# Optimization experiments

Hardware: AMD Instinct MI355X
Metric: run time of the kernel (lower is better)

Reference implementation:

```python
import jax, jax.numpy as jnp
import numpy as np

N_NODES = 100000
N_EDGES = 1600000
IN_DIM = 128
HID = 256
N_GRAPHS = 256
N_OUT = 2


def setup_inputs() -> dict:
    key = jax.random.key(0)
    ks = jax.random.split(key, 16)
    s_in = 1.0 / np.sqrt(IN_DIM)
    s_h = 1.0 / np.sqrt(HID)
    return {
        "x": jax.random.normal(ks[0], (N_NODES, IN_DIM), jnp.float32),
        "W_pool": jax.random.normal(ks[1], (IN_DIM, IN_DIM), jnp.float32) * s_in,
        "b_pool": jnp.zeros((IN_DIM,), jnp.float32),
        "W_self": jax.random.normal(ks[2], (IN_DIM, HID), jnp.float32) * s_in,
        "W_neigh": jax.random.normal(ks[3], (IN_DIM, HID), jnp.float32) * s_in,
        "b_sage": jnp.zeros((HID,), jnp.float32),
        "W1": jax.random.normal(ks[4], (HID, HID), jnp.float32) * s_h,
        "b1": jnp.zeros((HID,), jnp.float32),
        "W2": jax.random.normal(ks[5], (HID, HID), jnp.float32) * s_h,
        "b2": jnp.zeros((HID,), jnp.float32),
        "Wr": jax.random.normal(ks[6], (HID, N_OUT), jnp.float32) * s_h,
        "br": jnp.zeros((N_OUT,), jnp.float32),
        "src": jax.random.randint(ks[7], (N_EDGES,), 0, N_NODES, jnp.int32),
        "dst": jax.random.randint(ks[8], (N_EDGES,), 0, N_NODES, jnp.int32),
        "graph_id": jnp.sort(jax.random.randint(ks[9], (N_NODES,), 0, N_GRAPHS, jnp.int32)),
    }


def reference(x, W_pool, b_pool, W_self, W_neigh, b_sage, W1, b1, W2, b2, Wr, br, src, dst, graph_id):
    n = x.shape[0]
    # --- SAGEConv 'pool' aggregator ---
    m = jax.nn.relu(x @ W_pool + b_pool)                      # [N, IN]
    neigh = jax.ops.segment_max(m[src], dst, num_segments=n)  # max over in-neighbors
    neigh = jnp.where(jnp.isfinite(neigh), neigh, 0.0)        # isolated nodes -> 0 (DGL zero-init)
    h = jax.nn.relu(x @ W_self + neigh @ W_neigh + b_sage)    # [N, HID]
    # --- MLP stack ---
    h = jax.nn.relu(h @ W1 + b1)
    h = jax.nn.relu(h @ W2 + b2)
    # --- softmax_nodes: per-graph softmax over nodes, per feature ---
    gmax = jax.ops.segment_max(h, graph_id, num_segments=N_GRAPHS)
    gmax = jnp.where(jnp.isfinite(gmax), gmax, 0.0)
    z = jnp.exp(h - gmax[graph_id])                           # [N, HID]
    zsum = jax.ops.segment_sum(z, graph_id, num_segments=N_GRAPHS)
    hg = z / zsum[graph_id]
    # --- max_nodes readout ---
    final = jax.ops.segment_max(hg, graph_id, num_segments=N_GRAPHS)
    final = jnp.where(jnp.isfinite(final), final, 0.0)        # [G, HID]
    return final @ Wr + br                                    # [G, N_OUT]
```

## Files before the change

kernel.cpp:

```cpp
#include <hip/hip_runtime.h>

#define N_NODES  100000
#define N_EDGES  1600000
#define IN_DIM   128
#define HID      256
#define N_GRAPHS 256
#define ESHIFT   20.0f
#define BSH      7
#define NB2      782

typedef _Float16 f16x8 __attribute__((ext_vector_type(8)));
typedef float f32x16 __attribute__((ext_vector_type(16)));
#define MFMA16(a, b, c) __builtin_amdgcn_mfma_f32_32x32x16_f16((a), (b), (c), 0, 0, 0)

#define PKMAX(a, b) asm("v_pk_max_f16 %0, %0, %1" : "+v"(a) : "v"(b))

#define BARX() __builtin_amdgcn_s_barrier()
#define WAITVM(N) asm volatile("s_waitcnt vmcnt(" #N ")" ::: "memory")

static __device__ __forceinline__ unsigned short f2h_bits(float f) {
    _Float16 h = (_Float16)f;
    return __builtin_bit_cast(unsigned short, h);
}
static __device__ __forceinline__ float h2f(unsigned short b) {
    return (float)__builtin_bit_cast(_Float16, b);
}

static __device__ __forceinline__ void decode_blk(int M, int& m0, int& n0)
{
    const int gmb = (M + 127) >> 7;
    const int l = blockIdx.x;
    int mb, nb;
    if ((int)gridDim.x == gmb) {
        mb = l; nb = 0;
    } else {
        const int nfull = (gmb >> 3) << 4;
        if (l < nfull) {
            mb = ((l >> 4) << 3) | (l & 7);
            nb = (l >> 3) & 1;
        } else {
            const int t = l - nfull, tm = gmb & 7;
            mb = (gmb & ~7) + (t % tm);
            nb = t / tm;
        }
    }
    m0 = mb * 128;
    n0 = nb * 128;
}

__global__ __launch_bounds__(256) void x_to_h(
    const float* __restrict__ in, unsigned short* __restrict__ xh, int n)
{
    int i = (blockIdx.x * 256 + threadIdx.x) * 4;
    if (i < n) {
        float4 v = *(const float4*)&in[i];
        ushort4 h;
        h.x = f2h_bits(v.x); h.y = f2h_bits(v.y);
        h.z = f2h_bits(v.z); h.w = f2h_bits(v.w);
        *(ushort4*)&xh[i] = h;
    }
}

__global__ __launch_bounds__(256) void w_split_h(
    const float* __restrict__ Wa, const float* __restrict__ Wb, int K1,
    int K, int N, unsigned short* __restrict__ hi, unsigned short* __restrict__ lo)
{
    int idx = blockIdx.x * 256 + threadIdx.x;
    if (idx >= K * N) return;
    int k = idx / N, n = idx - k * N;
    float w = (k < K1) ? Wa[(size_t)k * N + n] : Wb[(size_t)(k - K1) * N + n];
    unsigned short h = f2h_bits(w);
    unsigned short l = f2h_bits(w - h2f(h));
    hi[(size_t)n * K + k] = h;
    lo[(size_t)n * K + k] = l;
}

__global__ __launch_bounds__(256) void gemm_mfma_h(
    const unsigned short* __restrict__ A1, const unsigned short* __restrict__ A2,
    int K1, int Ktot,
    const unsigned short* __restrict__ Wh, const unsigned short* __restrict__ Wl,
    const float* __restrict__ bias, void* __restrict__ Cv,
    int M, int N, int mode)
{
    __shared__ __align__(16) short tA [128][32];
    __shared__ __align__(16) short tBh[128][32];
    __shared__ __align__(16) short tBl[128][32];

    const int tid  = threadIdx.x;
    int m0, n0;
    decode_blk(M, m0, n0);
    const int wave = tid >> 6, lane = tid & 63;
    const int mw   = (wave & 1) * 64, nw = (wave >> 1) * 64;
    const int lm   = lane & 31;

    const int rsub = lane >> 2;
    const int kqe  = ((lane & 3) ^ ((lane >> 3) & 3)) << 3;
    const int rw   = wave << 5;

    const int s4  = (lm >> 1) & 3;
    const int cB  = lane >> 5;
    const int ch0 = ((cB ^ s4) << 3);
    const int ch1 = (((2 | cB) ^ s4) << 3);
    const f16x8* a00 = (const f16x8*)&tA [mw + lm     ][ch0];
    const f16x8* a01 = (const f16x8*)&tA [mw + lm     ][ch1];
    const f16x8* a10 = (const f16x8*)&tA [mw + 32 + lm][ch0];
    const f16x8* a11 = (const f16x8*)&tA [mw + 32 + lm][ch1];
    const f16x8* bh00 = (const f16x8*)&tBh[nw + lm     ][ch0];
    const f16x8* bh01 = (const f16x8*)&tBh[nw + lm     ][ch1];
    const f16x8* bh10 = (const f16x8*)&tBh[nw + 32 + lm][ch0];
    const f16x8* bh11 = (const f16x8*)&tBh[nw + 32 + lm][ch1];
    const f16x8* bl00 = (const f16x8*)&tBl[nw + lm     ][ch0];
    const f16x8* bl01 = (const f16x8*)&tBl[nw + lm     ][ch1];
    const f16x8* bl10 = (const f16x8*)&tBl[nw + 32 + lm][ch0];
    const f16x8* bl11 = (const f16x8*)&tBl[nw + 32 + lm][ch1];

    f32x16 acc[4];
#pragma unroll
    for (int t = 0; t < 4; ++t)
#pragma unroll
        for (int i = 0; i < 16; ++i) acc[t][i] = 0.f;

    for (int kc = 0; kc < Ktot; kc += 32) {
        const unsigned short* Ab; int Astr, kl;
        if (kc < K1) { Ab = A1; Astr = K1;        kl = kc; }
        else         { Ab = A2; Astr = Ktot - K1; kl = kc - K1; }

        __syncthreads();
#pragma unroll
        for (int j = 0; j < 2; ++j) {
            const int tr = rw + j * 16;
            int row = m0 + tr + rsub; if (row >= M) row = M - 1;
            __builtin_amdgcn_global_load_lds(
                Ab + (size_t)row * Astr + kl + kqe, &tA[tr][0], 16, 0, 0);
            const size_t o = (size_t)(n0 + tr + rsub) * Ktot + kc + kqe;
            __builtin_amdgcn_global_load_lds(Wh + o, &tBh[tr][0], 16, 0, 0);
            __builtin_amdgcn_global_load_lds(Wl + o, &tBl[tr][0], 16, 0, 0);
        }
        __syncthreads();

        {
            f16x8 A0 = *a00, A1f = *a10;
            f16x8 B0h = *bh00, B1h = *bh10, B0l = *bl00, B1l = *bl10;
            acc[0] = MFMA16(A0,  B0h, acc[0]);
            acc[1] = MFMA16(A0,  B1h, acc[1]);
            acc[2] = MFMA16(A1f, B0h, acc[2]);
            acc[3] = MFMA16(A1f, B1h, acc[3]);
            acc[0] = MFMA16(A0,  B0l, acc[0]);
            acc[1] = MFMA16(A0,  B1l, acc[1]);
            acc[2] = MFMA16(A1f, B0l, acc[2]);
            acc[3] = MFMA16(A1f, B1l, acc[3]);
        }
        {
            f16x8 A0 = *a01, A1f = *a11;
            f16x8 B0h = *bh01, B1h = *bh11, B0l = *bl01, B1l = *bl11;
            acc[0] = MFMA16(A0,  B0h, acc[0]);
            acc[1] = MFMA16(A0,  B1h, acc[1]);
            acc[2] = MFMA16(A1f, B0h, acc[2]);
            acc[3] = MFMA16(A1f, B1h, acc[3]);
            acc[0] = MFMA16(A0,  B0l, acc[0]);
            acc[1] = MFMA16(A0,  B1l, acc[1]);
            acc[2] = MFMA16(A1f, B0l, acc[2]);
            acc[3] = MFMA16(A1f, B1l, acc[3]);
        }
    }

    const int rb = 4 * (lane >> 5);
#pragma unroll
    for (int ti = 0; ti < 2; ++ti)
#pragma unroll
    for (int tj = 0; tj < 2; ++tj) {
        f32x16 a = acc[ti * 2 + tj];
        int coln = n0 + nw + tj * 32 + lm;
        float bv = bias[coln];
#pragma unroll
        for (int reg = 0; reg < 16; ++reg) {
            int rrow = m0 + mw + ti * 32 + (reg & 3) + 8 * (reg >> 2) + rb;
            if (rrow < M) {
                float v = a[reg] + bv;
                v = v > 0.f ? v : 0.f;
                size_t o = (size_t)rrow * N + coln;
                if (mode == 0) ((float*)Cv)[o] = v;
                else           ((unsigned short*)Cv)[o] = f2h_bits(v);
            }
        }
    }
}

static __device__ __forceinline__ void stage_tile64(
    const unsigned short* __restrict__ A1, const unsigned short* __restrict__ A2,
    int K1, int M, int r0g, short* bufb, int wave, int lane)
{
    const int l5 = lane >> 5;
    const int s  = lane & 31;
#pragma unroll
    for (int i = 0; i < 4; ++i) {
        const int p    = wave * 4 + i;
        const int rloc = 2 * p + l5;
        int row = r0g + rloc; if (row >= M) row = M - 1;
        const int c8 = ((s ^ ((2 * i + l5) & 7)) << 3);
        const unsigned short* sp = (c8 < K1)
            ? A1 + (size_t)row * K1 + c8
            : A2 + (size_t)row * (256 - K1) + (c8 - K1);
        __builtin_amdgcn_global_load_lds(sp, bufb + p * 512, 16, 0, 0);
    }
}

__global__ __launch_bounds__(512, 2) void gemm_bstat(
    const unsigned short* __restrict__ A1, const unsigned short* __restrict__ A2,
    int K1,
    const unsigned short* __restrict__ Wh, const unsigned short* __restrict__ Wl,
    const float* __restrict__ bias, unsigned short* __restrict__ C,
    unsigned short* __restrict__ dummy, int M)
{
    __shared__ __align__(16) short buf[2][64][256];

    const int tid = threadIdx.x, wave = tid >> 6, lane = tid & 63;
    const int lm = lane & 31, hib = lane >> 5;
    const int col = wave * 32 + lm;
    const int hi8 = hib * 8;

    f16x8 Bh[16], Bl[16];
#pragma unroll
    for (int k = 0; k < 16; ++k) {
        const size_t o = (size_t)col * 256 + k * 16 + hi8;
        Bh[k] = *(const f16x8*)(Wh + o);
        Bl[k] = *(const f16x8*)(Wl + o);
    }

    const int nt = (M + 63) >> 6;
    const int G = gridDim.x, b = blockIdx.x;
    const int q = nt / G, r = nt % G;
    const int t0  = b * q + (b < r ? b : r);
    const int ntl = q + (b < r ? 1 : 0);

    const int rq    = (lm >> 1) & 3;
    const int abase = lm * 512 + ((hib ^ (lm & 1)) << 4);
    const float bv  = bias[col];
    const int rb    = 4 * hib;

    stage_tile64(A1, A2, K1, M, t0 << 6, &buf[0][0][0], wave, lane);
    if (ntl > 1)
        stage_tile64(A1, A2, K1, M, (t0 + 1) << 6, &buf[1][0][0], wave, lane);

    for (int t = 0; t < ntl; ++t) {
        if (t == 0) { if (ntl > 1) WAITVM(4); else WAITVM(0); }
        else if (t + 1 < ntl) WAITVM(36);
        else WAITVM(32);
        BARX();

        f32x16 acc0, acc1;
#pragma unroll
        for (int i = 0; i < 16; ++i) { acc0[i] = 0.f; acc1[i] = 0.f; }
        const char* lb = (const char*)&buf[t & 1][0][0];
#pragma unroll
        for (int k = 0; k < 16; ++k) {
            const int koff = ((k ^ rq) << 5);
            f16x8 a0 = *(const f16x8*)(lb + abase + koff);
            f16x8 a1 = *(const f16x8*)(lb + abase + koff + 16384);
            acc0 = MFMA16(a0, Bh[k], acc0);
            acc1 = MFMA16(a1, Bh[k], acc1);
            acc0 = MFMA16(a0, Bl[k], acc0);
            acc1 = MFMA16(a1, Bl[k], acc1);
        }
        BARX();

        if (t + 2 < ntl)
            stage_tile64(A1, A2, K1, M, (t0 + t + 2) << 6,
                         &buf[t & 1][0][0], wave, lane);
        const int r0g = (t0 + t) << 6;
#pragma unroll
        for (int reg = 0; reg < 16; ++reg) {
            const int rr0 = r0g + (reg & 3) + 8 * (reg >> 2) + rb;
            const int rr1 = rr0 + 32;
            unsigned short* d0 = (rr0 < M) ? C + (size_t)rr0 * 256 + col : dummy + tid;
            unsigned short* d1 = (rr1 < M) ? C + (size_t)rr1 * 256 + col : dummy + tid;
            *d0 = f2h_bits(fmaxf(acc0[reg] + bv, 0.f));
            *d1 = f2h_bits(fmaxf(acc1[reg] + bv, 0.f));
        }
    }
}

static __device__ __forceinline__ void sm_flush(
    int run_g, float run_s, float run_m, int gfirst, int col,
    float* sS, int* sM, float* ps, float* pm)
{
    if (run_g < 0) return;
    int slot = run_g - gfirst;
    if (slot < 8) {
        atomicAdd(&sS[slot * 256 + col], run_s);
        atomicMax(&sM[slot * 256 + col], __float_as_int(run_m));
    } else {
        atomicAdd(&ps[(size_t)run_g * HID + col], run_s);
        atomicMax((int*)&pm[(size_t)run_g * HID + col], __float_as_int(run_m));
    }
}

__global__ __launch_bounds__(512, 2) void gemm_bstat_sm(
    const unsigned short* __restrict__ A,
    const unsigned short* __restrict__ Wh, const unsigned short* __restrict__ Wl,
    const float* __restrict__ bias, const int* __restrict__ gid,
    float* __restrict__ pm, float* __restrict__ ps, int M)
{
    __shared__ __align__(16) short buf[2][64][256];
    __shared__ float sS[8 * 256];
    __shared__ int   sM[8 * 256];

    const int tid = threadIdx.x, wave = tid >> 6, lane = tid & 63;
    const int lm = lane & 31, hib = lane >> 5;
    const int col = wave * 32 + lm;
    const int hi8 = hib * 8;

    for (int i = tid; i < 2048; i += 512) { sS[i] = 0.f; sM[i] = 0; }

    f16x8 Bh[16], Bl[16];
#pragma unroll
    for (int k = 0; k < 16; ++k) {
        const size_t o = (size_t)col * 256 + k * 16 + hi8;
        Bh[k] = *(const f16x8*)(Wh + o);
        Bl[k] = *(const f16x8*)(Wl + o);
    }

    const int nt = (M + 63) >> 6;
    const int G = gridDim.x, b = blockIdx.x;
    const int q = nt / G, r = nt % G;
    const int t0  = b * q + (b < r ? b : r);
    const int ntl = q + (b < r ? 1 : 0);

    const int rq    = (lm >> 1) & 3;
    const int abase = lm * 512 + ((hib ^ (lm & 1)) << 4);
    const float bv  = bias[col];
    const int rb    = 4 * hib;
    const int gfirst = gid[t0 << 6];

    stage_tile64(A, A, 256, M, t0 << 6, &buf[0][0][0], wave, lane);
    if (ntl > 1)
        stage_tile64(A, A, 256, M, (t0 + 1) << 6, &buf[1][0][0], wave, lane);

    int run_g = -1; float run_s = 0.f, run_m = 0.f;

    for (int t = 0; t < ntl; ++t) {
        if (t + 1 < ntl) WAITVM(4); else WAITVM(0);
        BARX();

        const int r0g = (t0 + t) << 6;
        int gr = r0g + lane; if (gr >= M) gr = M - 1;
        int gv = gid[gr];
        asm volatile("" :: "v"(gv));

        f32x16 acc0, acc1;
#pragma unroll
        for (int i = 0; i < 16; ++i) { acc0[i] = 0.f; acc1[i] = 0.f; }
        const char* lb = (const char*)&buf[t & 1][0][0];
#pragma unroll
        for (int k = 0; k < 16; ++k) {
            const int koff = ((k ^ rq) << 5);
            f16x8 a0 = *(const f16x8*)(lb + abase + koff);
            f16x8 a1 = *(const f16x8*)(lb + abase + koff + 16384);
            acc0 = MFMA16(a0, Bh[k], acc0);
            acc1 = MFMA16(a1, Bh[k], acc1);
            acc0 = MFMA16(a0, Bl[k], acc0);
            acc1 = MFMA16(a1, Bl[k], acc1);
        }
        BARX();

        if (t + 2 < ntl) {
            stage_tile64(A, A, 256, M, (t0 + t + 2) << 6,
                         &buf[t & 1][0][0], wave, lane);
            WAITVM(4);
        } else {
            WAITVM(0);
        }

        const int gT0 = __shfl(gv, 0);
        const int gT1 = __shfl(gv, 63);
        if (gT0 == gT1) {
            if (gT0 != run_g) {
                sm_flush(run_g, run_s, run_m, gfirst, col, sS, sM, ps, pm);
                run_g = gT0; run_s = 0.f; run_m = 0.f;
            }
#pragma unroll
            for (int sub = 0; sub < 2; ++sub) {
                const f32x16& a = sub ? acc1 : acc0;
#pragma unroll
                for (int reg = 0; reg < 16; ++reg) {
                    const int rrow = r0g + sub * 32 + (reg & 3) + 8 * (reg >> 2) + rb;
                    float v = fmaxf(a[reg] + bv, 0.f);
                    bool ok = rrow < M;
                    run_s += ok ? __expf(v - ESHIFT) : 0.f;
                    run_m = ok ? fmaxf(run_m, v) : run_m;
                }
            }
        } else {
#pragma unroll
            for (int sub = 0; sub < 2; ++sub) {
                const f32x16& a = sub ? acc1 : acc0;
#pragma unroll
                for (int reg = 0; reg < 16; ++reg) {
                    const int roff = sub * 32 + (reg & 3) + 8 * (reg >> 2) + rb;
                    const int rrow = r0g + roff;
                    int g = __shfl(gv, roff);
                    if (rrow >= M) continue;
                    float v = fmaxf(a[reg] + bv, 0.f);
                    if (g != run_g) {
                        sm_flush(run_g, run_s, run_m, gfirst, col, sS, sM, ps, pm);
                        run_g = g; run_s = 0.f; run_m = 0.f;
                    }
                    run_s += __expf(v - ESHIFT);
                    run_m = fmaxf(run_m, v);
                }
            }
        }
    }

    sm_flush(run_g, run_s, run_m, gfirst, col, sS, sM, ps, pm);
    __syncthreads();

    int lastrow = ((t0 + ntl) << 6) - 1; if (lastrow >= M) lastrow = M - 1;
    int span = gid[lastrow] - gfirst + 1; if (span > 8) span = 8;
    for (int i = tid; i < span * 256; i += 512) {
        float vs = sS[i];
        if (vs > 0.f) {
            int g = gfirst + (i >> 8), c = i & 255;
            atomicAdd(&ps[(size_t)g * HID + c], vs);
            atomicMax((int*)&pm[(size_t)g * HID + c], sM[i]);
        }
    }
}

__global__ __launch_bounds__(256) void part_count(
    const int* __restrict__ dst, int* __restrict__ btot, int E)
{
    __shared__ int sh[NB2];
    const int t = threadIdx.x;
    for (int i = t; i < NB2; i += 256) sh[i] = 0;
    __syncthreads();
    int base = blockIdx.x * 4096 + t;
#pragma unroll
    for (int i = 0; i < 16; ++i) {
        int e = base + i * 256;
        if (e < E) atomicAdd(&sh[dst[e] >> BSH], 1);
    }
    __syncthreads();
    for (int i = t; i < NB2; i += 256)
        if (sh[i]) atomicAdd(&btot[i], sh[i]);
}

__global__ __launch_bounds__(256) void scan_b(
    const int* __restrict__ btot, int* __restrict__ bstart,
    int* __restrict__ cursor, int total)
{
    __shared__ int sh[256];
    const int t = threadIdx.x;
    int a[4];
    int s = 0;
#pragma unroll
    for (int i = 0; i < 4; ++i) {
        int idx = t * 4 + i;
        a[i] = (idx < NB2) ? btot[idx] : 0;
        s += a[i];
    }
    sh[t] = s;
    __syncthreads();
    for (int off = 1; off < 256; off <<= 1) {
        int v = (t >= off) ? sh[t - off] : 0;
        __syncthreads();
        if (t >= off) sh[t] += v;
        __syncthreads();
    }
    int run = (t > 0) ? sh[t - 1] : 0;
#pragma unroll
    for (int i = 0; i < 4; ++i) {
        int idx = t * 4 + i;
        if (idx < NB2) { bstart[idx] = run; cursor[idx] = run; }
        run += a[i];
    }
    if (t == 0) bstart[NB2] = total;
}

__global__ __launch_bounds__(256) void part_scatter(
    const int* __restrict__ src, const int* __restrict__ dst,
    int* __restrict__ cursor, int2* __restrict__ pairs, int E)
{
    __shared__ int cnt[NB2], goff[NB2], fill[NB2];
    const int t = threadIdx.x;
    const int base = blockIdx.x * 4096;
    for (int i = t; i < NB2; i += 256) { cnt[i] = 0; fill[i] = 0; }
    __syncthreads();
    int myd[16];
#pragma unroll
    for (int i = 0; i < 16; ++i) {
        int e = base + t + i * 256;
        myd[i] = (e < E) ? dst[e] : -1;
        if (myd[i] >= 0) atomicAdd(&cnt[myd[i] >> BSH], 1);
    }
    __syncthreads();
    for (int i = t; i < NB2; i += 256)
        goff[i] = cnt[i] ? atomicAdd(&cursor[i], cnt[i]) : 0;
    __syncthreads();
#pragma unroll
    for (int i = 0; i < 16; ++i) {
        int e = base + t + i * 256;
        if (myd[i] >= 0) {
            int b = myd[i] >> BSH;
            int r = atomicAdd(&fill[b], 1);
            pairs[goff[b] + r] = make_int2(myd[i], src[e]);
        }
    }
}

__global__ __launch_bounds__(256) void bucket_sort(
    const int2* __restrict__ pairs, const int* __restrict__ bstart,
    int* __restrict__ csr_src, int* __restrict__ offs, int Nn, int E)
{
    __shared__ int cnt[128], off[128];
    const int b = blockIdx.x;
    const int t = threadIdx.x;
    const int lo = bstart[b], hi = bstart[b + 1];
    if (t < 128) cnt[t] = 0;
    __syncthreads();
    for (int e = lo + t; e < hi; e += 256)
        atomicAdd(&cnt[pairs[e].x & 127], 1);
    __syncthreads();
    if (t == 0) {
        int s = 0;
        for (int i = 0; i < 128; ++i) { off[i] = s; s += cnt[i]; }
    }
    __syncthreads();
    if (t < 128) {
        int node = (b << BSH) + t;
        if (node < Nn) offs[node] = lo + off[t];
        cnt[t] = off[t];
    }
    if (b == NB2 - 1 && t == 0) offs[Nn] = E;
    __syncthreads();
    for (int e = lo + t; e < hi; e += 256) {
        int2 p = pairs[e];
        int r = atomicAdd(&cnt[p.x & 127], 1);
        csr_src[lo + r] = p.y;
    }
}

__global__ __launch_bounds__(256) void csr_max_agg_h(
    const unsigned short* __restrict__ m, const int* __restrict__ csr_src,
    const int* __restrict__ offs, unsigned short* __restrict__ neigh, int Nn)
{
    const int node = (blockIdx.x * 256 + threadIdx.x) >> 6;
    const int lane = threadIdx.x & 63;
    if (node >= Nn) return;
    const int e0  = offs[node];
    const int end = offs[node + 1];
    const char* mc = (const char*)m;

    uint4 a0 = make_uint4(0u, 0u, 0u, 0u);
    uint4 a1 = a0, a2 = a0, a3 = a0;
    if (end > e0) {
        const unsigned fo = (unsigned)(lane & 15) << 4;
        const int sub = lane >> 4;
        for (int base = e0; base < end; base += 64) {
            int ee = base + lane;
            int sl = csr_src[ee < end ? ee : (end - 1)];
            int cnt = end - base; if (cnt > 64) cnt = 64;
            int iters = (cnt + 3) >> 2;
            for (int j = 0; j < iters; j += 4) {
                int j1 = j + 1 < 16 ? j + 1 : 15;
                int j2 = j + 2 < 16 ? j + 2 : 15;
                int j3 = j + 3 < 16 ? j + 3 : 15;
                int s0 = __shfl(sl, (j  << 2) | sub);
                int s1 = __shfl(sl, (j1 << 2) | sub);
                int s2 = __shfl(sl, (j2 << 2) | sub);
                int s3 = __shfl(sl, (j3 << 2) | sub);
                uint4 v0 = *(const uint4*)(mc + (((unsigned)s0 << 8) | fo));
                uint4 v1 = *(const uint4*)(mc + (((unsigned)s1 << 8) | fo));
                uint4 v2 = *(const uint4*)(mc + (((unsigned)s2 << 8) | fo));
                uint4 v3 = *(const uint4*)(mc + (((unsigned)s3 << 8) | fo));
                PKMAX(a0.x, v0.x); PKMAX(a0.y, v0.y);
                PKMAX(a0.z, v0.z); PKMAX(a0.w, v0.w);
                PKMAX(a1.x, v1.x); PKMAX(a1.y, v1.y);
                PKMAX(a1.z, v1.z); PKMAX(a1.w, v1.w);
                PKMAX(a2.x, v2.x); PKMAX(a2.y, v2.y);
                PKMAX(a2.z, v2.z); PKMAX(a2.w, v2.w);
                PKMAX(a3.x, v3.x); PKMAX(a3.y, v3.y);
                PKMAX(a3.z, v3.z); PKMAX(a3.w, v3.w);
            }
        }
        PKMAX(a0.x, a1.x); PKMAX(a0.y, a1.y);
        PKMAX(a0.z, a1.z); PKMAX(a0.w, a1.w);
        PKMAX(a2.x, a3.x); PKMAX(a2.y, a3.y);
        PKMAX(a2.z, a3.z); PKMAX(a2.w, a3.w);
        PKMAX(a0.x, a2.x); PKMAX(a0.y, a2.y);
        PKMAX(a0.z, a2.z); PKMAX(a0.w, a2.w);
        uint4 o;
        o.x = __shfl_xor(a0.x, 16); o.y = __shfl_xor(a0.y, 16);
        o.z = __shfl_xor(a0.z, 16); o.w = __shfl_xor(a0.w, 16);
        PKMAX(a0.x, o.x); PKMAX(a0.y, o.y);
        PKMAX(a0.z, o.z); PKMAX(a0.w, o.w);
        o.x = __shfl_xor(a0.x, 32); o.y = __shfl_xor(a0.y, 32);
        o.z = __shfl_xor(a0.z, 32); o.w = __shfl_xor(a0.w, 32);
        PKMAX(a0.x, o.x); PKMAX(a0.y, o.y);
        PKMAX(a0.z, o.z); PKMAX(a0.w, o.w);
    }
    if (lane < 16)
        *(uint4*)((char*)neigh + (((size_t)node << 8) | ((unsigned)lane << 4))) = a0;
}

__global__ __launch_bounds__(256) void softmax_merge(
    const float* __restrict__ pm, const float* __restrict__ ps,
    const float* __restrict__ Wr, const float* __restrict__ brv,
    float* __restrict__ out)
{
    const int g = blockIdx.x;
    const int j = threadIdx.x;

    float M = pm[(size_t)g * HID + j];
    float S = ps[(size_t)g * HID + j];
    float fm = (S > 0.f) ? __expf(M - ESHIFT) / S : 0.f;

    float p0 = fm * Wr[j * 2 + 0];
    float p1 = fm * Wr[j * 2 + 1];
#pragma unroll
    for (int off = 32; off > 0; off >>= 1) {
        p0 += __shfl_down(p0, off);
        p1 += __shfl_down(p1, off);
    }
    __shared__ float red[8];
    int wv = j >> 6, ln = j & 63;
    if (ln == 0) { red[wv * 2] = p0; red[wv * 2 + 1] = p1; }
    __syncthreads();
    if (j == 0) out[g * 2 + 0] = red[0] + red[2] + red[4] + red[6] + brv[0];
    if (j == 1) out[g * 2 + 1] = red[1] + red[3] + red[5] + red[7] + brv[1];
}

extern "C" void kernel_launch(void* const* d_in, const int* in_sizes, int n_in,
                              void* d_out, int out_size, void* d_ws, size_t ws_size,
                              hipStream_t stream)
{
    const float* x      = (const float*)d_in[0];
    const float* W_pool = (const float*)d_in[1];
    const float* b_pool = (const float*)d_in[2];
    const float* W_self = (const float*)d_in[3];
    const float* W_neigh= (const float*)d_in[4];
    const float* b_sage = (const float*)d_in[5];
    const float* W1     = (const float*)d_in[6];
    const float* b1     = (const float*)d_in[7];
    const float* W2     = (const float*)d_in[8];
    const float* b2     = (const float*)d_in[9];
    const float* Wr     = (const float*)d_in[10];
    const float* br     = (const float*)d_in[11];
    const int*   src    = (const int*)d_in[12];
    const int*   dst    = (const int*)d_in[13];
    const int*   gid    = (const int*)d_in[14];

    const int Nn = N_NODES, E = N_EDGES;
    char* ws = (char*)d_ws;

    unsigned short* xh    = (unsigned short*)(ws + 0);
    unsigned short* m_buf = (unsigned short*)(ws + 25600000);
    unsigned short* neigh = (unsigned short*)(ws + 51200000);
    int2*           pairs = (int2*)(ws + 76800000);
    int*            btot  = (int*)(ws + 89600000);
    int*            bstart= btot + NB2;
    int*            cursor= bstart + NB2 + 1;
    float*          pm    = (float*)(ws + 90000000);
    float*          ps    = pm + (size_t)N_GRAPHS * HID;
    int*            offs  = (int*)(ws + 91000000);
    int*            csr_src = (int*)(ws + 91500000);
    unsigned short* h1    = (unsigned short*)(ws + 102400000);
    unsigned short* h2    = (unsigned short*)(ws + 153600000);
    unsigned short* dummy = (unsigned short*)pairs;

    char* srcws = (char*)(void*)src;
    unsigned short* wpool_h = (unsigned short*)(srcws + 0);
    unsigned short* wpool_l = wpool_h + 128 * 128;
    unsigned short* wsage_h = wpool_l + 128 * 128;
    unsigned short* wsage_l = wsage_h + 256 * 256;
    unsigned short* w1_h    = wsage_l + 256 * 256;
    unsigned short* w1_l    = w1_h + 256 * 256;
    unsigned short* w2_h    = w1_l + 256 * 256;
    unsigned short* w2_l    = w2_h + 256 * 256;

    dim3 blk(256);
    const int gm = (Nn + 127) / 128;
    const int pchunks = (E + 4095) / 4096;

    hipMemsetAsync(btot, 0, NB2 * sizeof(int), stream);
    hipMemsetAsync(pm, 0, (size_t)2 * N_GRAPHS * HID * sizeof(float), stream);

    x_to_h<<<dim3((Nn * IN_DIM / 4 + 255) / 256), blk, 0, stream>>>(
        x, xh, Nn * IN_DIM);

    part_count<<<dim3(pchunks), blk, 0, stream>>>(dst, btot, E);
    scan_b<<<dim3(1), blk, 0, stream>>>(btot, bstart, cursor, E);
    part_scatter<<<dim3(pchunks), blk, 0, stream>>>(src, dst, cursor, pairs, E);
    bucket_sort<<<dim3(NB2), blk, 0, stream>>>(pairs, bstart, csr_src, offs, Nn, E);

    w_split_h<<<dim3((128 * 128 + 255) / 256), blk, 0, stream>>>(
        W_pool, W_pool, 128, 128, 128, wpool_h, wpool_l);
    w_split_h<<<dim3((256 * 256 + 255) / 256), blk, 0, stream>>>(
        W_self, W_neigh, 128, 256, 256, wsage_h, wsage_l);
    w_split_h<<<dim3((256 * 256 + 255) / 256), blk, 0, stream>>>(
        W1, W1, 256, 256, 256, w1_h, w1_l);
    w_split_h<<<dim3((256 * 256 + 255) / 256), blk, 0, stream>>>(
        W2, W2, 256, 256, 256, w2_h, w2_l);

    gemm_mfma_h<<<dim3(gm), blk, 0, stream>>>(
        xh, xh, 128, 128, wpool_h, wpool_l, b_pool, m_buf, Nn, 128, 1);

    csr_max_agg_h<<<dim3((Nn * 64 + 255) / 256), blk, 0, stream>>>(
        m_buf, csr_src, offs, neigh, Nn);

    gemm_bstat<<<dim3(256), dim3(512), 0, stream>>>(
        xh, neigh, 128, wsage_h, wsage_l, b_sage, h1, dummy, Nn);

    gemm_bstat<<<dim3(256), dim3(512), 0, stream>>>(
        h1, h1, 256, w1_h, w1_l, b1, h2, dummy, Nn);

    gemm_bstat_sm<<<dim3(256), dim3(512), 0, stream>>>(
        h2, w2_h, w2_l, b2, gid, pm, ps, Nn);

    softmax_merge<<<dim3(N_GRAPHS), blk, 0, stream>>>(pm, ps, Wr, br, (float*)d_out);
}
```

Before: 411.8 us.

## Fuse prep kernels and use persistent register-resident-weight GEMM for pool layer

Merges the x-to-fp16 conversion with the edge-bucket counting into one launch, and the four weight-split launches into one. It also replaces the generic LDS-tiled GEMM for the pool projection with a persistent 256-block kernel. That kernel keeps the 128x128 hi/lo weights in registers and double-buffers 64-row A tiles through LDS. The aim is to cut launch overhead and the redundant weight loads per tile in the first GEMM, at the cost of higher register pressure and manual vmcnt bookkeeping.

```diff
diff --git a/kernel.cpp b/kernel.cpp
--- a/kernel.cpp
+++ b/kernel.cpp
@@ -8,6 +8,7 @@
 #define ESHIFT   20.0f
 #define BSH      7
 #define NB2      782
+#define XHB      12500
 
 typedef _Float16 f16x8 __attribute__((ext_vector_type(8)));
 typedef float f32x16 __attribute__((ext_vector_type(16)));
@@ -26,46 +27,41 @@
     return (float)__builtin_bit_cast(_Float16, b);
 }
 
-static __device__ __forceinline__ void decode_blk(int M, int& m0, int& n0)
-{
-    const int gmb = (M + 127) >> 7;
-    const int l = blockIdx.x;
-    int mb, nb;
-    if ((int)gridDim.x == gmb) {
-        mb = l; nb = 0;
-    } else {
-        const int nfull = (gmb >> 3) << 4;
-        if (l < nfull) {
-            mb = ((l >> 4) << 3) | (l & 7);
-            nb = (l >> 3) & 1;
-        } else {
-            const int t = l - nfull, tm = gmb & 7;
-            mb = (gmb & ~7) + (t % tm);
-            nb = t / tm;
-        }
-    }
-    m0 = mb * 128;
-    n0 = nb * 128;
-}
-
-__global__ __launch_bounds__(256) void x_to_h(
-    const float* __restrict__ in, unsigned short* __restrict__ xh, int n)
-{
-    int i = (blockIdx.x * 256 + threadIdx.x) * 4;
-    if (i < n) {
-        float4 v = *(const float4*)&in[i];
-        ushort4 h;
-        h.x = f2h_bits(v.x); h.y = f2h_bits(v.y);
-        h.z = f2h_bits(v.z); h.w = f2h_bits(v.w);
-        *(ushort4*)&xh[i] = h;
-    }
-}
-
-__global__ __launch_bounds__(256) void w_split_h(
+__global__ __launch_bounds__(256) void prep_xh_count(
+    const float* __restrict__ x, unsigned short* __restrict__ xh, int nx,
+    const int* __restrict__ dst, int* __restrict__ btot, int E)
+{
+    __shared__ int sh[NB2];
+    const int t = threadIdx.x;
+    if ((int)blockIdx.x < XHB) {
+        int i = (blockIdx.x * 256 + t) * 4;
+        if (i < nx) {
+            float4 v = *(const float4*)&x[i];
+            ushort4 h;
+            h.x = f2h_bits(v.x); h.y = f2h_bits(v.y);
+            h.z = f2h_bits(v.z); h.w = f2h_bits(v.w);
+            *(ushort4*)&xh[i] = h;
+        }
+        return;
+    }
+    for (int i = t; i < NB2; i += 256) sh[i] = 0;
+    __syncthreads();
+    int base = (blockIdx.x - XHB) * 4096 + t;
+#pragma unroll
+    for (int i = 0; i < 16; ++i) {
+        int e = base + i * 256;
+        if (e < E) atomicAdd(&sh[dst[e] >> BSH], 1);
+    }
+    __syncthreads();
+    for (int i = t; i < NB2; i += 256)
+        if (sh[i]) atomicAdd(&btot[i], sh[i]);
+}
+
+static __device__ __forceinline__ void wsplit_seg(
     const float* __restrict__ Wa, const float* __restrict__ Wb, int K1,
-    int K, int N, unsigned short* __restrict__ hi, unsigned short* __restrict__ lo)
-{
-    int idx = blockIdx.x * 256 + threadIdx.x;
+    int K, int N, unsigned short* __restrict__ hi, unsigned short* __restrict__ lo,
+    int idx)
+{
     if (idx >= K * N) return;
     int k = idx / N, n = idx - k * N;
     float w = (k < K1) ? Wa[(size_t)k * N + n] : Wb[(size_t)(k - K1) * N + n];
@@ -75,115 +71,28 @@
     lo[(size_t)n * K + k] = l;
 }
 
-__global__ __launch_bounds__(256) void gemm_mfma_h(
-    const unsigned short* __restrict__ A1, const unsigned short* __restrict__ A2,
-    int K1, int Ktot,
-    const unsigned short* __restrict__ Wh, const unsigned short* __restrict__ Wl,
-    const float* __restrict__ bias, void* __restrict__ Cv,
-    int M, int N, int mode)
-{
-    __shared__ __align__(16) short tA [128][32];
-    __shared__ __align__(16) short tBh[128][32];
-    __shared__ __align__(16) short tBl[128][32];
-
-    const int tid  = threadIdx.x;
-    int m0, n0;
-    decode_blk(M, m0, n0);
-    const int wave = tid >> 6, lane = tid & 63;
-    const int mw   = (wave & 1) * 64, nw = (wave >> 1) * 64;
-    const int lm   = lane & 31;
-
-    const int rsub = lane >> 2;
-    const int kqe  = ((lane & 3) ^ ((lane >> 3) & 3)) << 3;
-    const int rw   = wave << 5;
-
-    const int s4  = (lm >> 1) & 3;
-    const int cB  = lane >> 5;
-    const int ch0 = ((cB ^ s4) << 3);
-    const int ch1 = (((2 | cB) ^ s4) << 3);
-    const f16x8* a00 = (const f16x8*)&tA [mw + lm     ][ch0];
-    const f16x8* a01 = (const f16x8*)&tA [mw + lm     ][ch1];
-    const f16x8* a10 = (const f16x8*)&tA [mw + 32 + lm][ch0];
-    const f16x8* a11 = (const f16x8*)&tA [mw + 32 + lm][ch1];
-    const f16x8* bh00 = (const f16x8*)&tBh[nw + lm     ][ch0];
-    const f16x8* bh01 = (const f16x8*)&tBh[nw + lm     ][ch1];
-    const f16x8* bh10 = (const f16x8*)&tBh[nw + 32 + lm][ch0];
-    const f16x8* bh11 = (const f16x8*)&tBh[nw + 32 + lm][ch1];
-    const f16x8* bl00 = (const f16x8*)&tBl[nw + lm     ][ch0];
-    const f16x8* bl01 = (const f16x8*)&tBl[nw + lm     ][ch1];
-    const f16x8* bl10 = (const f16x8*)&tBl[nw + 32 + lm][ch0];
-    const f16x8* bl11 = (const f16x8*)&tBl[nw + 32 + lm][ch1];
-
-    f32x16 acc[4];
-#pragma unroll
-    for (int t = 0; t < 4; ++t)
-#pragma unroll
-        for (int i = 0; i < 16; ++i) acc[t][i] = 0.f;
-
-    for (int kc = 0; kc < Ktot; kc += 32) {
-        const unsigned short* Ab; int Astr, kl;
-        if (kc < K1) { Ab = A1; Astr = K1;        kl = kc; }
-        else         { Ab = A2; Astr = Ktot - K1; kl = kc - K1; }
-
-        __syncthreads();
-#pragma unroll
-        for (int j = 0; j < 2; ++j) {
-            const int tr = rw + j * 16;
-            int row = m0 + tr + rsub; if (row >= M) row = M - 1;
-            __builtin_amdgcn_global_load_lds(
-                Ab + (size_t)row * Astr + kl + kqe, &tA[tr][0], 16, 0, 0);
-            const size_t o = (size_t)(n0 + tr + rsub) * Ktot + kc + kqe;
-            __builtin_amdgcn_global_load_lds(Wh + o, &tBh[tr][0], 16, 0, 0);
-            __builtin_amdgcn_global_load_lds(Wl + o, &tBl[tr][0], 16, 0, 0);
-        }
-        __syncthreads();
-
-        {
-            f16x8 A0 = *a00, A1f = *a10;
-            f16x8 B0h = *bh00, B1h = *bh10, B0l = *bl00, B1l = *bl10;
-            acc[0] = MFMA16(A0,  B0h, acc[0]);
-            acc[1] = MFMA16(A0,  B1h, acc[1]);
-            acc[2] = MFMA16(A1f, B0h, acc[2]);
-            acc[3] = MFMA16(A1f, B1h, acc[3]);
-            acc[0] = MFMA16(A0,  B0l, acc[0]);
-            acc[1] = MFMA16(A0,  B1l, acc[1]);
-            acc[2] = MFMA16(A1f, B0l, acc[2]);
-            acc[3] = MFMA16(A1f, B1l, acc[3]);
-        }
-        {
-            f16x8 A0 = *a01, A1f = *a11;
-            f16x8 B0h = *bh01, B1h = *bh11, B0l = *bl01, B1l = *bl11;
-            acc[0] = MFMA16(A0,  B0h, acc[0]);
-            acc[1] = MFMA16(A0,  B1h, acc[1]);
-            acc[2] = MFMA16(A1f, B0h, acc[2]);
-            acc[3] = MFMA16(A1f, B1h, acc[3]);
-            acc[0] = MFMA16(A0,  B0l, acc[0]);
-            acc[1] = MFMA16(A0,  B1l, acc[1]);
-            acc[2] = MFMA16(A1f, B0l, acc[2]);
-            acc[3] = MFMA16(A1f, B1l, acc[3]);
-        }
-    }
-
-    const int rb = 4 * (lane >> 5);
-#pragma unroll
-    for (int ti = 0; ti < 2; ++ti)
-#pragma unroll
-    for (int tj = 0; tj < 2; ++tj) {
-        f32x16 a = acc[ti * 2 + tj];
-        int coln = n0 + nw + tj * 32 + lm;
-        float bv = bias[coln];
-#pragma unroll
-        for (int reg = 0; reg < 16; ++reg) {
-            int rrow = m0 + mw + ti * 32 + (reg & 3) + 8 * (reg >> 2) + rb;
-            if (rrow < M) {
-                float v = a[reg] + bv;
-                v = v > 0.f ? v : 0.f;
-                size_t o = (size_t)rrow * N + coln;
-                if (mode == 0) ((float*)Cv)[o] = v;
-                else           ((unsigned short*)Cv)[o] = f2h_bits(v);
-            }
-        }
-    }
+__global__ __launch_bounds__(256) void w_split_all(
+    const float* __restrict__ Wp, const float* __restrict__ Ws,
+    const float* __restrict__ Wn, const float* __restrict__ W1,
+    const float* __restrict__ W2, unsigned short* __restrict__ base)
+{
+    const int blk = blockIdx.x, tid = threadIdx.x;
+    unsigned short* wpool_h = base;
+    unsigned short* wpool_l = wpool_h + 16384;
+    unsigned short* wsage_h = wpool_l + 16384;
+    unsigned short* wsage_l = wsage_h + 65536;
+    unsigned short* w1_h    = wsage_l + 65536;
+    unsigned short* w1_l    = w1_h + 65536;
+    unsigned short* w2_h    = w1_l + 65536;
+    unsigned short* w2_l    = w2_h + 65536;
+    if (blk < 64)
+        wsplit_seg(Wp, Wp, 128, 128, 128, wpool_h, wpool_l, blk * 256 + tid);
+    else if (blk < 320)
+        wsplit_seg(Ws, Wn, 128, 256, 256, wsage_h, wsage_l, (blk - 64) * 256 + tid);
+    else if (blk < 576)
+        wsplit_seg(W1, W1, 256, 256, 256, w1_h, w1_l, (blk - 320) * 256 + tid);
+    else
+        wsplit_seg(W2, W2, 256, 256, 256, w2_h, w2_l, (blk - 576) * 256 + tid);
 }
 
 static __device__ __forceinline__ void stage_tile64(
@@ -276,6 +185,87 @@
             unsigned short* d1 = (rr1 < M) ? C + (size_t)rr1 * 256 + col : dummy + tid;
             *d0 = f2h_bits(fmaxf(acc0[reg] + bv, 0.f));
             *d1 = f2h_bits(fmaxf(acc1[reg] + bv, 0.f));
+        }
+    }
+}
+
+static __device__ __forceinline__ void stage_tile64_k128(
+    const unsigned short* __restrict__ A, int M, int r0g,
+    short* bufb, int wave, int lane)
+{
+#pragma unroll
+    for (int p = 0; p < 2; ++p) {
+        const int rl = p * 32 + wave * 4 + (lane >> 4);
+        int row = r0g + rl; if (row >= M) row = M - 1;
+        const int ch = (lane & 15) ^ (rl & 7);
+        __builtin_amdgcn_global_load_lds(
+            A + (size_t)row * 128 + ch * 8,
+            bufb + p * 4096 + wave * 512, 16, 0, 0);
+    }
+}
+
+__global__ __launch_bounds__(512, 2) void gemm_bstat128(
+    const unsigned short* __restrict__ A,
+    const unsigned short* __restrict__ Wh, const unsigned short* __restrict__ Wl,
+    const float* __restrict__ bias, unsigned short* __restrict__ C,
+    unsigned short* __restrict__ dummy, int M)
+{
+    __shared__ __align__(16) short buf[2][64][128];
+
+    const int tid = threadIdx.x, wave = tid >> 6, lane = tid & 63;
+    const int lm = lane & 31, hib = lane >> 5;
+    const int colT = wave & 3;
+    const int rw   = (wave >> 2) * 32;
+    const int col  = colT * 32 + lm;
+
+    f16x8 Bh[8], Bl[8];
+#pragma unroll
+    for (int k = 0; k < 8; ++k) {
+        const size_t o = (size_t)col * 128 + k * 16 + hib * 8;
+        Bh[k] = *(const f16x8*)(Wh + o);
+        Bl[k] = *(const f16x8*)(Wl + o);
+    }
+
+    const int nt = (M + 63) >> 6;
+    const int G = gridDim.x, b = blockIdx.x;
+    const int q = nt / G, r = nt % G;
+    const int t0  = b * q + (b < r ? b : r);
+    const int ntl = q + (b < r ? 1 : 0);
+
+    const int ch0 = hib ^ (lm & 7);
+    const float bv = bias[col];
+
+    stage_tile64_k128(A, M, t0 << 6, &buf[0][0][0], wave, lane);
+    if (ntl > 1)
+        stage_tile64_k128(A, M, (t0 + 1) << 6, &buf[1][0][0], wave, lane);
+
+    for (int t = 0; t < ntl; ++t) {
+        if (t == 0) { if (ntl > 1) WAITVM(2); else WAITVM(0); }
+        else if (t + 1 < ntl) WAITVM(18);
+        else WAITVM(16);
+        BARX();
+
+        f32x16 acc;
+#pragma unroll
+        for (int i = 0; i < 16; ++i) acc[i] = 0.f;
+        const char* lb = (const char*)&buf[t & 1][0][0] + (rw + lm) * 256;
+#pragma unroll
+        for (int k = 0; k < 8; ++k) {
+            f16x8 a = *(const f16x8*)(lb + (((2 * k) ^ ch0) << 4));
+            acc = MFMA16(a, Bh[k], acc);
+            acc = MFMA16(a, Bl[k], acc);
+        }
+        BARX();
+
+        if (t + 2 < ntl)
+            stage_tile64_k128(A, M, (t0 + t + 2) << 6,
+                              &buf[t & 1][0][0], wave, lane);
+        const int r0g = (t0 + t) << 6;
+#pragma unroll
+        for (int reg = 0; reg < 16; ++reg) {
+            const int rr = r0g + rw + (reg & 3) + 8 * (reg >> 2) + 4 * hib;
+            unsigned short* d = (rr < M) ? C + (size_t)rr * 128 + col : dummy + tid;
+            *d = f2h_bits(fmaxf(acc[reg] + bv, 0.f));
         }
     }
 }
@@ -425,24 +415,6 @@
             atomicMax((int*)&pm[(size_t)g * HID + c], sM[i]);
         }
     }
-}
-
-__global__ __launch_bounds__(256) void part_count(
-    const int* __restrict__ dst, int* __restrict__ btot, int E)
-{
-    __shared__ int sh[NB2];
-    const int t = threadIdx.x;
-    for (int i = t; i < NB2; i += 256) sh[i] = 0;
-    __syncthreads();
-    int base = blockIdx.x * 4096 + t;
-#pragma unroll
-    for (int i = 0; i < 16; ++i) {
-        int e = base + i * 256;
-        if (e < E) atomicAdd(&sh[dst[e] >> BSH], 1);
-    }
-    __syncthreads();
-    for (int i = t; i < NB2; i += 256)
-        if (sh[i]) atomicAdd(&btot[i], sh[i]);
 }
 
 __global__ __launch_bounds__(256) void scan_b(
@@ -679,31 +651,24 @@
     unsigned short* w2_l    = w2_h + 256 * 256;
 
     dim3 blk(256);
-    const int gm = (Nn + 127) / 128;
     const int pchunks = (E + 4095) / 4096;
 
     hipMemsetAsync(btot, 0, NB2 * sizeof(int), stream);
     hipMemsetAsync(pm, 0, (size_t)2 * N_GRAPHS * HID * sizeof(float), stream);
 
-    x_to_h<<<dim3((Nn * IN_DIM / 4 + 255) / 256), blk, 0, stream>>>(
-        x, xh, Nn * IN_DIM);
-
-    part_count<<<dim3(pchunks), blk, 0, stream>>>(dst, btot, E);
+    prep_xh_count<<<dim3(XHB + pchunks), blk, 0, stream>>>(
+        x, xh, Nn * IN_DIM, dst, btot, E);
+
     scan_b<<<dim3(1), blk, 0, stream>>>(btot, bstart, cursor, E);
     part_scatter<<<dim3(pchunks), blk, 0, stream>>>(src, dst, cursor, pairs, E);
+
+    w_split_all<<<dim3(832), blk, 0, stream>>>(
+        W_pool, W_self, W_neigh, W1, W2, (unsigned short*)srcws);
+
     bucket_sort<<<dim3(NB2), blk, 0, stream>>>(pairs, bstart, csr_src, offs, Nn, E);
 
-    w_split_h<<<dim3((128 * 128 + 255) / 256), blk, 0, stream>>>(
-        W_pool, W_pool, 128, 128, 128, wpool_h, wpool_l);
-    w_split_h<<<dim3((256 * 256 + 255) / 256), blk, 0, stream>>>(
-        W_self, W_neigh, 128, 256, 256, wsage_h, wsage_l);
-    w_split_h<<<dim3((256 * 256 + 255) / 256), blk, 0, stream>>>(
-        W1, W1, 256, 256, 256, w1_h, w1_l);
-    w_split_h<<<dim3((256 * 256 + 255) / 256), blk, 0, stream>>>(
-        W2, W2, 256, 256, 256, w2_h, w2_l);
-
-    gemm_mfma_h<<<dim3(gm), blk, 0, stream>>>(
-        xh, xh, 128, 128, wpool_h, wpool_l, b_pool, m_buf, Nn, 128, 1);
+    gemm_bstat128<<<dim3(256), dim3(512), 0, stream>>>(
+        xh, wpool_h, wpool_l, b_pool, m_buf, dummy, Nn);
 
     csr_max_agg_h<<<dim3((Nn * 64 + 255) / 256), blk, 0, stream>>>(
         m_buf, csr_src, offs, neigh, Nn);
```

After: 395.2 us, median of 2. 4.0% less time.
